# Performance work log

Measured on AMD Instinct MI355X. Metric: run time of the kernel, lower is better.

The kernel has to match this reference:

```python
import jax, jax.numpy as jnp
import numpy as np

B, N, D, L, NREPEAT = 32, 577, 384, 12, 4
H = 4 * D  # mlp hidden
EPS = 1e-6


def ln(x, w, b):
    mu = jnp.mean(x, axis=-1, keepdims=True)
    var = jnp.mean(jnp.square(x - mu), axis=-1, keepdims=True)
    return (x - mu) * jax.lax.rsqrt(var + EPS) * w + b


def setup_inputs() -> dict:
    key = jax.random.key(0)
    ks = jax.random.split(key, 16)
    s = 0.02
    return {
        "x": jax.random.normal(ks[0], (B, N, D), dtype=jnp.float32),
        "norm1_w": jnp.ones((L, D), jnp.float32),
        "norm1_b": jnp.zeros((L, D), jnp.float32),
        "qkv_w": jax.random.normal(ks[1], (L, 3 * D, D), jnp.float32) * s,
        "qkv_b": jnp.zeros((L, 3 * D), jnp.float32),
        "qn_w": jnp.ones((L, D), jnp.float32),
        "qn_b": jnp.zeros((L, D), jnp.float32),
        "kn_w": jnp.ones((L, D), jnp.float32),
        "kn_b": jnp.zeros((L, D), jnp.float32),
        "an_w": jnp.ones((L, D), jnp.float32),
        "an_b": jnp.zeros((L, D), jnp.float32),
        "proj_w": jax.random.normal(ks[2], (L, D, D), jnp.float32) * s,
        "proj_b": jnp.zeros((L, D), jnp.float32),
        "ls1": jnp.full((L, D), 1e-5, jnp.float32),
        "norm2_w": jnp.ones((L, D), jnp.float32),
        "norm2_b": jnp.zeros((L, D), jnp.float32),
        "fc1_w": jax.random.normal(ks[3], (L, H, D), jnp.float32) * s,
        "fc1_b": jnp.zeros((L, H), jnp.float32),
        "fc2_w": jax.random.normal(ks[4], (L, D, H), jnp.float32) * s,
        "fc2_b": jnp.zeros((L, D), jnp.float32),
        "ls2": jnp.full((L, D), 1e-5, jnp.float32),
    }


def _forward(x, norm1_w, norm1_b, qkv_w, qkv_b, qn_w, qn_b, kn_w, kn_b,
             an_w, an_b, proj_w, proj_b, ls1, norm2_w, norm2_b,
             fc1_w, fc1_b, fc2_w, fc2_b, ls2):
    scale = 1.0 / np.sqrt(D).astype(np.float32)
    x_prime = x
    history = []  # list of [B, 1, D] cls tokens, grows each repeat
    for _ in range(NREPEAT):
        new_cls = x[:, 0:1]
        x = jnp.concatenate([new_cls, x_prime[:, 1:]], axis=1)  # [B, N, D]
        mem = jnp.concatenate([x] + history, axis=1)            # [B, N+t, D]
        for l in range(L):
            res1 = x
            xn = ln(x, norm1_w[l], norm1_b[l])
            # manual qkv split: q from normed x, k/v from UNNORMED mem
            q = xn @ qkv_w[l, :D].T + qkv_b[l, :D]
            k = mem @ qkv_w[l, D:2 * D].T + qkv_b[l, D:2 * D]
            v = mem @ qkv_w[l, 2 * D:].T + qkv_b[l, 2 * D:]
            q = ln(q, qn_w[l], qn_b[l])
            k = ln(k, kn_w[l], kn_b[l])
            # single-head SDPA over full width D
            attn = jax.nn.softmax(jnp.einsum('bqd,bkd->bqk', q, k) * scale, axis=-1)
            prod = jnp.einsum('bqk,bkd->bqd', attn, v)
            prod = ln(prod, an_w[l], an_b[l])
            proj = prod @ proj_w[l].T + proj_b[l]
            x = proj * ls1[l] + res1
            res2 = x
            x2 = ln(x, norm2_w[l], norm2_b[l])
            h = jax.nn.gelu(x2 @ fc1_w[l].T + fc1_b[l], approximate=False)
            x1 = h @ fc2_w[l].T + fc2_b[l]
            x = x1 * ls2[l] + res2
        history.append(new_cls)
    return x


def reference(x, norm1_w, norm1_b, qkv_w, qkv_b, qn_w, qn_b, kn_w, kn_b,
              an_w, an_b, proj_w, proj_b, ls1, norm2_w, norm2_b,
              fc1_w, fc1_b, fc2_w, fc2_b, ls2):
    return _forward(x, norm1_w, norm1_b, qkv_w, qkv_b, qn_w, qn_b, kn_w, kn_b,
                    an_w, an_b, proj_w, proj_b, ls1, norm2_w, norm2_b,
                    fc1_w, fc1_b, fc2_w, fc2_b, ls2)
```

## Files before the change

### kernel.cpp

```cpp
#include <hip/hip_runtime.h>
#include <math.h>

#define BB 32
#define NN 577
#define DD 384
#define HD 1536
#define LL 12
#define MP 640
#define NRPT 4

typedef __attribute__((ext_vector_type(8))) short bf16x8;
typedef __attribute__((ext_vector_type(4))) float f32x4;

__device__ __forceinline__ unsigned short f2bf(float f){
  unsigned u = __builtin_bit_cast(unsigned, f);
  u += 0x7fffu + ((u >> 16) & 1u);
  return (unsigned short)(u >> 16);
}
__device__ __forceinline__ float bf2f(unsigned short s){
  unsigned u = ((unsigned)s) << 16;
  return __builtin_bit_cast(float, u);
}

__device__ __forceinline__ void async16(void* lds, const void* g){
  __builtin_amdgcn_global_load_lds(
      (const __attribute__((address_space(1))) unsigned int*)g,
      (__attribute__((address_space(3))) unsigned int*)lds, 16, 0, 0);
}

__global__ void prep_k(float* __restrict__ x, const float* __restrict__ xp,
                       float* __restrict__ cls_r, const float* __restrict__ cls_hist,
                       unsigned short* __restrict__ mem, int r){
  int i = blockIdx.x * 256 + threadIdx.x;
  if (i >= BB*MP*DD) return;
  int d = i % DD;
  int n = (i / DD) % MP;
  int b = i / (MP*DD);
  float v;
  if (n == 0){ v = x[(size_t)b*NN*DD + d]; cls_r[b*DD + d] = v; }
  else if (n < NN){ v = xp[((size_t)b*NN + n)*DD + d]; x[((size_t)b*NN + n)*DD + d] = v; }
  else if (n < NN + r){ v = cls_hist[(size_t)(n-NN)*BB*DD + b*DD + d]; }
  else v = 0.f;
  mem[i] = f2bf(v);
}

__global__ void castL_k(const float* __restrict__ qkvw, const float* __restrict__ pw,
                        const float* __restrict__ f1w, const float* __restrict__ f2w,
                        unsigned short* __restrict__ wbuf){
  int i = blockIdx.x * 256 + threadIdx.x;
  const int QKV = 3*DD*DD;
  const int PRJ = DD*DD;
  const int F1  = HD*DD;
  const int TOT = QKV + PRJ + 2*F1;
  if (i >= TOT) return;
  float v;
  if (i < QKV) v = qkvw[i];
  else if (i < QKV+PRJ) v = pw[i-QKV];
  else if (i < QKV+PRJ+F1) v = f1w[i-QKV-PRJ];
  else v = f2w[i-QKV-PRJ-F1];
  wbuf[i] = f2bf(v);
}

template<typename T>
__global__ __launch_bounds__(256) void ln4_k(const T* __restrict__ in, const float* __restrict__ w,
                                             const float* __restrict__ bias, unsigned short* __restrict__ out,
                                             int nrows){
  int row = blockIdx.x*4 + (threadIdx.x >> 6);
  if (row >= nrows) return;
  int lane = threadIdx.x & 63;
  const T* p = in + (size_t)row*DD;
  float v[6];
  float s = 0.f;
  #pragma unroll
  for (int i=0;i<6;i++){
    float t;
    if (sizeof(T) == 4) t = (float)p[lane + i*64];
    else t = bf2f((unsigned short)p[lane + i*64]);
    v[i] = t; s += t;
  }
  #pragma unroll
  for (int o=32;o;o>>=1) s += __shfl_xor(s, o, 64);
  float mu = s * (1.f/DD);
  float q = 0.f;
  #pragma unroll
  for (int i=0;i<6;i++){ float t = v[i]-mu; q += t*t; }
  #pragma unroll
  for (int o=32;o;o>>=1) q += __shfl_xor(q, o, 64);
  float rs = rsqrtf(q*(1.f/DD) + 1e-6f);
  unsigned short* po = out + (size_t)row*DD;
  #pragma unroll
  for (int i=0;i<6;i++){
    int c = lane + i*64;
    po[c] = f2bf((v[i]-mu)*rs*w[c] + bias[c]);
  }
}

__global__ __launch_bounds__(256) void lnqk_k(const unsigned short* __restrict__ qraw,
                                              const unsigned short* __restrict__ kraw,
                                              const float* __restrict__ qw, const float* __restrict__ qbias,
                                              const float* __restrict__ kw, const float* __restrict__ kbias,
                                              unsigned short* __restrict__ qo, unsigned short* __restrict__ ko){
  const int QR = BB*NN;
  int row = blockIdx.x*4 + (threadIdx.x >> 6);
  int lane = threadIdx.x & 63;
  bool isq = row < QR;
  const unsigned short* p = isq ? qraw + (size_t)row*DD : kraw + (size_t)(row-QR)*DD;
  const float* w  = isq ? qw : kw;
  const float* bs = isq ? qbias : kbias;
  unsigned short* po = isq ? qo + (size_t)row*DD : ko + (size_t)(row-QR)*DD;
  float scale = isq ? 0.05103103588f : 1.0f;
  float v[6];
  float s = 0.f;
  #pragma unroll
  for (int i=0;i<6;i++){ float t = bf2f(p[lane + i*64]); v[i] = t; s += t; }
  #pragma unroll
  for (int o=32;o;o>>=1) s += __shfl_xor(s, o, 64);
  float mu = s * (1.f/DD);
  float q = 0.f;
  #pragma unroll
  for (int i=0;i<6;i++){ float t = v[i]-mu; q += t*t; }
  #pragma unroll
  for (int o=32;o;o>>=1) q += __shfl_xor(q, o, 64);
  float rs = rsqrtf(q*(1.f/DD) + 1e-6f);
  #pragma unroll
  for (int i=0;i<6;i++){
    int c = lane + i*64;
    po[c] = f2bf(((v[i]-mu)*rs*w[c] + bs[c]) * scale);
  }
}

template<int EPI>
__global__ __launch_bounds__(256) void gemm128(
    const unsigned short* __restrict__ A, int lda, int arows, long sA,
    const unsigned short* __restrict__ B, int ldb, int brows, long sB,
    const float* __restrict__ bias,
    int K, int N,
    float* __restrict__ outF, unsigned short* __restrict__ outB,
    int ldo, int orows, long sO,
    const float* __restrict__ ls){

  __shared__ unsigned short a_sh[2][128*32];
  __shared__ unsigned short b_sh[2][128*32];

  int tid  = threadIdx.x;
  int wave = tid >> 6, lane = tid & 63;
  int lr = lane & 15, kg = lane >> 4;
  int wm = wave >> 1, wn = wave & 1;
  int z = blockIdx.z;
  int row0 = blockIdx.y * 128;
  int col0 = blockIdx.x * 128;

  const unsigned short* Ab = A + (size_t)z*sA;
  const unsigned short* Bb = B + (size_t)z*sB;

  f32x4 zf = {0.f,0.f,0.f,0.f};
  f32x4 acc[4][4];
  #pragma unroll
  for (int i=0;i<4;i++)
    #pragma unroll
    for (int j=0;j<4;j++) acc[i][j] = zf;

  int ra[2], rb[2], kc[2];
  #pragma unroll
  for (int it=0; it<2; it++){
    int c = tid + it*256;
    int r = row0 + (c>>2); if (r > arows-1) r = arows-1;
    ra[it] = r;
    r = col0 + (c>>2); if (r > brows-1) r = brows-1;
    rb[it] = r;
    kc[it] = (c&3)*8;
  }

  for (int k0 = 0; k0 < K; k0 += 64){
    #pragma unroll
    for (int p=0;p<2;p++){
      #pragma unroll
      for (int it=0; it<2; it++){
        unsigned short* la = &a_sh[p][(it*256 + wave*64)*8];
        unsigned short* lb = &b_sh[p][(it*256 + wave*64)*8];
        async16(la, Ab + (size_t)ra[it]*lda + k0 + p*32 + kc[it]);
        async16(lb, Bb + (size_t)rb[it]*ldb + k0 + p*32 + kc[it]);
      }
    }
    __syncthreads();
    #pragma unroll
    for (int p=0;p<2;p++){
      bf16x8 af[4], bfr[4];
      #pragma unroll
      for (int i=0;i<4;i++){
        af[i]  = *(const bf16x8*)&a_sh[p][(wm*64 + i*16 + lr)*32 + kg*8];
        bfr[i] = *(const bf16x8*)&b_sh[p][(wn*64 + i*16 + lr)*32 + kg*8];
      }
      #pragma unroll
      for (int i=0;i<4;i++)
        #pragma unroll
        for (int j=0;j<4;j++)
          acc[i][j] = __builtin_amdgcn_mfma_f32_16x16x32_bf16(af[i], bfr[j], acc[i][j], 0,0,0);
    }
    __syncthreads();
  }

  float* oF = outF ? outF + (size_t)z*sO : nullptr;
  unsigned short* oB = outB ? outB + (size_t)z*sO : nullptr;

  #pragma unroll
  for (int mi=0;mi<4;mi++)
    #pragma unroll
    for (int ni=0;ni<4;ni++)
      #pragma unroll
      for (int r=0;r<4;r++){
        int row = row0 + wm*64 + mi*16 + kg*4 + r;
        int col = col0 + wn*64 + ni*16 + lr;
        if (row >= orows || col >= N) continue;
        float vv = acc[mi][ni][r];
        size_t idx = (size_t)row*ldo + col;
        if (EPI == 0){
          if (bias) vv += bias[col];
          oB[idx] = f2bf(vv);
        } else if (EPI == 1){
          vv += bias[row];
          oB[idx] = f2bf(vv);
        } else if (EPI == 2){
          vv += bias[col];
          oF[idx] = vv*ls[col] + oF[idx];
        } else {
          vv += bias[col];
          float g = 0.5f*vv*(1.f + erff(vv*0.70710678118f));
          oB[idx] = f2bf(g);
        }
      }
}

__global__ __launch_bounds__(256, 2) void attn_k(
    const unsigned short* __restrict__ qs,
    const unsigned short* __restrict__ kb,
    const unsigned short* __restrict__ vT,
    const float* __restrict__ anw, const float* __restrict__ anb,
    unsigned short* __restrict__ out, int M){

  __shared__ unsigned short k_sh[32*384];
  __shared__ unsigned short v_sh[384*32];
  __shared__ unsigned short p_sh[64*56];

  int tid = threadIdx.x;
  int wv = tid >> 6, lane = tid & 63;
  int lr = lane & 15, kg = lane >> 4;
  int b = blockIdx.y, qt0 = blockIdx.x * 64;

  bf16x8 qf[12];
  {
    int qrow = qt0 + wv*16 + lr; if (qrow > NN-1) qrow = NN-1;
    const unsigned short* qp = qs + ((size_t)b*NN + qrow)*DD;
    #pragma unroll
    for (int ks=0; ks<12; ks++) qf[ks] = *(const bf16x8*)(qp + ks*32 + kg*8);
  }

  f32x4 zf = {0.f,0.f,0.f,0.f};
  f32x4 O[24];
  #pragma unroll
  for (int i=0;i<24;i++) O[i] = zf;
  float m_run[4], l_run[4];
  #pragma unroll
  for (int r=0;r<4;r++){ m_run[r] = -INFINITY; l_run[r] = 0.f; }

  for (int kt=0; kt<19; kt++){
    __syncthreads();
    #pragma unroll
    for (int i=0;i<6;i++){
      int L = i*256 + tid;
      int row = L/48, c = L%48;
      int gc = (c & ~7) | ((c ^ row) & 7);
      async16(&k_sh[L*8], kb + ((size_t)b*MP + kt*32 + row)*DD + gc*8);
    }
    #pragma unroll
    for (int i=0;i<6;i++){
      int L = i*256 + tid;
      int row = L>>2;
      int gc = (L&3) ^ (row&3);
      async16(&v_sh[L*8], vT + ((size_t)b*DD + row)*MP + kt*32 + gc*8);
    }
    __syncthreads();

    f32x4 s[2] = {zf, zf};
    #pragma unroll
    for (int ks=0; ks<12; ks++){
      int c = ks*4 + kg;
      #pragma unroll
      for (int nk=0; nk<2; nk++){
        int krow = nk*16 + lr;
        bf16x8 bk = *(const bf16x8*)&k_sh[krow*DD + ((c & ~7) | ((c ^ krow)&7))*8];
        s[nk] = __builtin_amdgcn_mfma_f32_16x16x32_bf16(qf[ks], bk, s[nk], 0,0,0);
      }
    }
    #pragma unroll
    for (int nk=0; nk<2; nk++){
      if (kt*32 + nk*16 + lr >= M){
        s[nk][0] = -INFINITY; s[nk][1] = -INFINITY; s[nk][2] = -INFINITY; s[nk][3] = -INFINITY;
      }
    }
    float al[4];
    #pragma unroll
    for (int r=0;r<4;r++){
      float v = fmaxf(s[0][r], s[1][r]);
      v = fmaxf(v, __shfl_xor(v, 1, 64));
      v = fmaxf(v, __shfl_xor(v, 2, 64));
      v = fmaxf(v, __shfl_xor(v, 4, 64));
      v = fmaxf(v, __shfl_xor(v, 8, 64));
      float mn = fmaxf(m_run[r], v);
      al[r] = __expf(m_run[r] - mn);
      m_run[r] = mn;
    }
    #pragma unroll
    for (int nk=0;nk<2;nk++)
      #pragma unroll
      for (int r=0;r<4;r++)
        s[nk][r] = __expf(s[nk][r] - m_run[r]);
    #pragma unroll
    for (int r=0;r<4;r++){
      float v = s[0][r] + s[1][r];
      v += __shfl_xor(v, 1, 64);
      v += __shfl_xor(v, 2, 64);
      v += __shfl_xor(v, 4, 64);
      v += __shfl_xor(v, 8, 64);
      l_run[r] = al[r]*l_run[r] + v;
    }
    #pragma unroll
    for (int nk=0;nk<2;nk++)
      #pragma unroll
      for (int r=0;r<4;r++)
        p_sh[(wv*16 + kg*4 + r)*56 + nk*16 + lr] = f2bf(s[nk][r]);
    #pragma unroll
    for (int ni=0;ni<24;ni++)
      #pragma unroll
      for (int r=0;r<4;r++) O[ni][r] *= al[r];
    __syncthreads();

    bf16x8 ap = *(const bf16x8*)&p_sh[(wv*16 + lr)*56 + kg*8];
    #pragma unroll
    for (int ni=0;ni<24;ni++){
      int d = ni*16 + lr;
      bf16x8 bv = *(const bf16x8*)&v_sh[d*32 + ((kg ^ (d&3))*8)];
      O[ni] = __builtin_amdgcn_mfma_f32_16x16x32_bf16(ap, bv, O[ni], 0,0,0);
    }
  }

  float inv[4];
  #pragma unroll
  for (int r=0;r<4;r++) inv[r] = 1.f / l_run[r];
  float s1[4] = {0,0,0,0}, s2[4] = {0,0,0,0};
  #pragma unroll
  for (int ni=0;ni<24;ni++)
    #pragma unroll
    for (int r=0;r<4;r++){
      float x = O[ni][r]*inv[r];
      O[ni][r] = x;
      s1[r] += x; s2[r] += x*x;
    }
  #pragma unroll
  for (int r=0;r<4;r++){
    #pragma unroll
    for (int o=1;o<16;o<<=1){ s1[r] += __shfl_xor(s1[r], o, 64); s2[r] += __shfl_xor(s2[r], o, 64); }
  }
  float mu[4], rs[4];
  #pragma unroll
  for (int r=0;r<4;r++){
    mu[r] = s1[r]*(1.f/DD);
    float var = s2[r]*(1.f/DD) - mu[r]*mu[r];
    rs[r] = rsqrtf(fmaxf(var, 0.f) + 1e-6f);
  }
  int rowb = qt0 + wv*16 + kg*4;
  #pragma unroll
  for (int ni=0;ni<24;ni++){
    int col = ni*16 + lr;
    float wc = anw[col], bc = anb[col];
    #pragma unroll
    for (int r=0;r<4;r++){
      int qrow = rowb + r;
      if (qrow < NN)
        out[((size_t)b*NN + qrow)*DD + col] = f2bf((O[ni][r]-mu[r])*rs[r]*wc + bc);
    }
  }
}


extern "C" void kernel_launch(void* const* d_in, const int* in_sizes, int n_in,
                              void* d_out, int out_size, void* d_ws, size_t ws_size,
                              hipStream_t stream){
  const float* x_in = (const float*)d_in[0];
  const float* n1w  = (const float*)d_in[1];
  const float* n1b  = (const float*)d_in[2];
  const float* qkvw = (const float*)d_in[3];
  const float* qkvb = (const float*)d_in[4];
  const float* qnw  = (const float*)d_in[5];
  const float* qnb  = (const float*)d_in[6];
  const float* knw  = (const float*)d_in[7];
  const float* knb  = (const float*)d_in[8];
  const float* anw  = (const float*)d_in[9];
  const float* anb  = (const float*)d_in[10];
  const float* pw   = (const float*)d_in[11];
  const float* pb   = (const float*)d_in[12];
  const float* ls1  = (const float*)d_in[13];
  const float* n2w  = (const float*)d_in[14];
  const float* n2b  = (const float*)d_in[15];
  const float* f1w  = (const float*)d_in[16];
  const float* f1b  = (const float*)d_in[17];
  const float* f2w  = (const float*)d_in[18];
  const float* f2bb = (const float*)d_in[19];
  const float* ls2  = (const float*)d_in[20];

  char* ws = (char*)d_ws;
  size_t off = 0;
  auto alloc = [&](size_t bytes)->char* {
    char* p = ws + off;
    off = (off + bytes + 255) & ~(size_t)255;
    return p;
  };

  const int QKV = 3*DD*DD, PRJ = DD*DD, F1 = HD*DD;
  const size_t WTOT = (size_t)QKV + PRJ + 2*F1;
  const size_t SLOT = (size_t)BB*MP*DD;

  unsigned short* wbuf  = (unsigned short*)alloc(WTOT*2);
  float*          cls_h = (float*)         alloc((size_t)NRPT*BB*DD*4);
  unsigned short* mem_bf= (unsigned short*)alloc(SLOT*2);
  unsigned short* pool  = (unsigned short*)alloc(6*SLOT*2);

  unsigned short* wq = wbuf;
  unsigned short* wp = wbuf + QKV;
  unsigned short* w1 = wbuf + QKV + PRJ;
  unsigned short* w2 = wbuf + QKV + PRJ + F1;

  unsigned short* S0 = pool;
  unsigned short* S1 = pool + SLOT;
  unsigned short* S2 = pool + 2*SLOT;
  unsigned short* S3 = pool + 3*SLOT;
  unsigned short* S4 = pool + 4*SLOT;
  unsigned short* S5 = pool + 5*SLOT;

  unsigned short* xn    = S0;
  unsigned short* qraw  = S1;
  unsigned short* kraw  = S2;
  unsigned short* qb    = S3;
  unsigned short* kb    = S4;
  unsigned short* vT    = S5;
  unsigned short* prodn = S1;
  unsigned short* x2    = S0;
  unsigned short* h     = S1;

  float* xf = (float*)d_out;

  auto cg = [](size_t n){ return dim3((unsigned)((n + 255) / 256)); };

  hipMemcpyAsync(xf, x_in, (size_t)BB*NN*DD*4, hipMemcpyDeviceToDevice, stream);

  const int RT  = (BB*NN + 127)/128;
  const int RTM = (BB*MP)/128;
  const int QR  = BB*NN;
  const int KR  = BB*MP;

  for (int r = 0; r < NRPT; r++){
    int M = NN + r;
    prep_k<<<cg((size_t)BB*MP*DD),256,0,stream>>>(xf, x_in, cls_h + (size_t)r*BB*DD, cls_h, mem_bf, r);
    for (int l = 0; l < LL; l++){
      castL_k<<<cg(WTOT),256,0,stream>>>(qkvw + (size_t)l*QKV, pw + (size_t)l*PRJ,
                                         f1w + (size_t)l*F1, f2w + (size_t)l*F1, wbuf);
      ln4_k<float><<<cg((size_t)QR*64),256,0,stream>>>(xf, n1w + l*DD, n1b + l*DD, xn, QR);
      gemm128<0><<<dim3(3,RT,1),256,0,stream>>>(xn,384,QR,0, wq,384,384,0,
          qkvb + l*3*DD, 384,384, nullptr,qraw,384,QR,0, nullptr);
      gemm128<0><<<dim3(3,RTM,1),256,0,stream>>>(mem_bf,384,KR,0, wq + (size_t)DD*DD,384,384,0,
          qkvb + l*3*DD + DD, 384,384, nullptr,kraw,384,KR,0, nullptr);
      gemm128<1><<<dim3(MP/128,3,BB),256,0,stream>>>(wq + (size_t)2*DD*DD,384,384,0, mem_bf,384,MP,(long)MP*DD,
          qkvb + l*3*DD + 2*DD, 384,MP, nullptr,vT,MP,384,(long)DD*MP, nullptr);
      lnqk_k<<<(QR+KR)/4,256,0,stream>>>(qraw, kraw, qnw + l*DD, qnb + l*DD,
                                         knw + l*DD, knb + l*DD, qb, kb);
      attn_k<<<dim3(10,BB),256,0,stream>>>(qb, kb, vT, anw + l*DD, anb + l*DD, prodn, M);
      gemm128<2><<<dim3(3,RT,1),256,0,stream>>>(prodn,384,QR,0, wp,384,384,0,
          pb + l*DD, 384,384, xf,nullptr,384,QR,0, ls1 + l*DD);
      ln4_k<float><<<cg((size_t)QR*64),256,0,stream>>>(xf, n2w + l*DD, n2b + l*DD, x2, QR);
      gemm128<3><<<dim3(HD/128,RT,1),256,0,stream>>>(x2,384,QR,0, w1,384,HD,0,
          f1b + l*HD, 384,HD, nullptr,h,HD,QR,0, nullptr);
      gemm128<2><<<dim3(3,RT,1),256,0,stream>>>(h,HD,QR,0, w2,HD,384,0,
          f2bb + l*DD, HD,384, xf,nullptr,384,QR,0, ls2 + l*DD);
    }
  }
}
```

Measured before the change: 16.88 ms.

## Merge Q/K GEMMs, hoist weight casts, vectorize LN-QK, drop attention barrier

Merges the Q and K projection GEMMs into a single launch by placing xn and mem_bf contiguously, with blocks past a row split switching to the K weights and bias. Weight casting to bf16 now runs once per layer up front into a 12-layer buffer, rather than once per repeat per layer, whenever the workspace is large enough. lnqk_k loads and stores bf16 pairs as 32-bit words, and attention shrinks the P tile stride. It also removes a __syncthreads before reading P, which relies on each wave reading only its own rows, and any cross-wave hazard there would be a correctness risk.

```diff
diff --git a/kernel.cpp b/kernel.cpp
--- a/kernel.cpp
+++ b/kernel.cpp
@@ -8,6 +8,9 @@
 #define LL 12
 #define MP 640
 #define NRPT 4
+#define QR (BB*NN)
+#define QP 18560
+#define KR (BB*MP)
 
 typedef __attribute__((ext_vector_type(8))) short bf16x8;
 typedef __attribute__((ext_vector_type(4))) float f32x4;
@@ -61,23 +64,17 @@
   wbuf[i] = f2bf(v);
 }
 
-template<typename T>
-__global__ __launch_bounds__(256) void ln4_k(const T* __restrict__ in, const float* __restrict__ w,
+__global__ __launch_bounds__(256) void ln4_k(const float* __restrict__ in, const float* __restrict__ w,
                                              const float* __restrict__ bias, unsigned short* __restrict__ out,
                                              int nrows){
   int row = blockIdx.x*4 + (threadIdx.x >> 6);
   if (row >= nrows) return;
   int lane = threadIdx.x & 63;
-  const T* p = in + (size_t)row*DD;
+  const float* p = in + (size_t)row*DD;
   float v[6];
   float s = 0.f;
   #pragma unroll
-  for (int i=0;i<6;i++){
-    float t;
-    if (sizeof(T) == 4) t = (float)p[lane + i*64];
-    else t = bf2f((unsigned short)p[lane + i*64]);
-    v[i] = t; s += t;
-  }
+  for (int i=0;i<6;i++){ float t = p[lane + i*64]; v[i] = t; s += t; }
   #pragma unroll
   for (int o=32;o;o>>=1) s += __shfl_xor(s, o, 64);
   float mu = s * (1.f/DD);
@@ -100,19 +97,22 @@
                                               const float* __restrict__ qw, const float* __restrict__ qbias,
                                               const float* __restrict__ kw, const float* __restrict__ kbias,
                                               unsigned short* __restrict__ qo, unsigned short* __restrict__ ko){
-  const int QR = BB*NN;
   int row = blockIdx.x*4 + (threadIdx.x >> 6);
   int lane = threadIdx.x & 63;
   bool isq = row < QR;
-  const unsigned short* p = isq ? qraw + (size_t)row*DD : kraw + (size_t)(row-QR)*DD;
+  const unsigned int* p = (const unsigned int*)(isq ? qraw + (size_t)row*DD : kraw + (size_t)(row-QR)*DD);
   const float* w  = isq ? qw : kw;
   const float* bs = isq ? qbias : kbias;
-  unsigned short* po = isq ? qo + (size_t)row*DD : ko + (size_t)(row-QR)*DD;
+  unsigned int* po = (unsigned int*)(isq ? qo + (size_t)row*DD : ko + (size_t)(row-QR)*DD);
   float scale = isq ? 0.05103103588f : 1.0f;
   float v[6];
   float s = 0.f;
   #pragma unroll
-  for (int i=0;i<6;i++){ float t = bf2f(p[lane + i*64]); v[i] = t; s += t; }
+  for (int i=0;i<3;i++){
+    unsigned u = p[lane + i*64];
+    float a = bf2f((unsigned short)u), b = bf2f((unsigned short)(u>>16));
+    v[2*i] = a; v[2*i+1] = b; s += a + b;
+  }
   #pragma unroll
   for (int o=32;o;o>>=1) s += __shfl_xor(s, o, 64);
   float mu = s * (1.f/DD);
@@ -123,9 +123,11 @@
   for (int o=32;o;o>>=1) q += __shfl_xor(q, o, 64);
   float rs = rsqrtf(q*(1.f/DD) + 1e-6f);
   #pragma unroll
-  for (int i=0;i<6;i++){
-    int c = lane + i*64;
-    po[c] = f2bf(((v[i]-mu)*rs*w[c] + bs[c]) * scale);
+  for (int i=0;i<3;i++){
+    int c0 = 2*(lane + i*64);
+    unsigned short lo = f2bf(((v[2*i]  -mu)*rs*w[c0]   + bs[c0]  ) * scale);
+    unsigned short hi = f2bf(((v[2*i+1]-mu)*rs*w[c0+1] + bs[c0+1]) * scale);
+    po[lane + i*64] = (unsigned)lo | ((unsigned)hi << 16);
   }
 }
 
@@ -137,7 +139,9 @@
     int K, int N,
     float* __restrict__ outF, unsigned short* __restrict__ outB,
     int ldo, int orows, long sO,
-    const float* __restrict__ ls){
+    const float* __restrict__ ls,
+    int rowSplit, const unsigned short* __restrict__ B2,
+    const float* __restrict__ bias2, int orows2){
 
   __shared__ unsigned short a_sh[2][128*32];
   __shared__ unsigned short b_sh[2][128*32];
@@ -150,8 +154,13 @@
   int row0 = blockIdx.y * 128;
   int col0 = blockIdx.x * 128;
 
+  bool second = row0 >= rowSplit;
+  const unsigned short* Bu = second ? B2 : B;
+  const float* biasu = second ? bias2 : bias;
+  int limit = second ? orows2 : orows;
+
   const unsigned short* Ab = A + (size_t)z*sA;
-  const unsigned short* Bb = B + (size_t)z*sB;
+  const unsigned short* Bb = Bu + (size_t)z*sB;
 
   f32x4 zf = {0.f,0.f,0.f,0.f};
   f32x4 acc[4][4];
@@ -211,20 +220,20 @@
       for (int r=0;r<4;r++){
         int row = row0 + wm*64 + mi*16 + kg*4 + r;
         int col = col0 + wn*64 + ni*16 + lr;
-        if (row >= orows || col >= N) continue;
+        if (row >= limit || col >= N) continue;
         float vv = acc[mi][ni][r];
         size_t idx = (size_t)row*ldo + col;
         if (EPI == 0){
-          if (bias) vv += bias[col];
+          if (biasu) vv += biasu[col];
           oB[idx] = f2bf(vv);
         } else if (EPI == 1){
-          vv += bias[row];
+          vv += biasu[row];
           oB[idx] = f2bf(vv);
         } else if (EPI == 2){
-          vv += bias[col];
+          vv += biasu[col];
           oF[idx] = vv*ls[col] + oF[idx];
         } else {
-          vv += bias[col];
+          vv += biasu[col];
           float g = 0.5f*vv*(1.f + erff(vv*0.70710678118f));
           oB[idx] = f2bf(g);
         }
@@ -240,7 +249,7 @@
 
   __shared__ unsigned short k_sh[32*384];
   __shared__ unsigned short v_sh[384*32];
-  __shared__ unsigned short p_sh[64*56];
+  __shared__ unsigned short p_sh[64*40];
 
   int tid = threadIdx.x;
   int wv = tid >> 6, lane = tid & 63;
@@ -328,14 +337,13 @@
     for (int nk=0;nk<2;nk++)
       #pragma unroll
       for (int r=0;r<4;r++)
-        p_sh[(wv*16 + kg*4 + r)*56 + nk*16 + lr] = f2bf(s[nk][r]);
+        p_sh[(wv*16 + kg*4 + r)*40 + nk*16 + lr] = f2bf(s[nk][r]);
     #pragma unroll
     for (int ni=0;ni<24;ni++)
       #pragma unroll
       for (int r=0;r<4;r++) O[ni][r] *= al[r];
-    __syncthreads();
-
-    bf16x8 ap = *(const bf16x8*)&p_sh[(wv*16 + lr)*56 + kg*8];
+
+    bf16x8 ap = *(const bf16x8*)&p_sh[(wv*16 + lr)*40 + kg*8];
     #pragma unroll
     for (int ni=0;ni<24;ni++){
       int d = ni*16 + lr;
@@ -419,31 +427,31 @@
   const int QKV = 3*DD*DD, PRJ = DD*DD, F1 = HD*DD;
   const size_t WTOT = (size_t)QKV + PRJ + 2*F1;
   const size_t SLOT = (size_t)BB*MP*DD;
+  const size_t XNSZ = (size_t)QP*DD;
 
   unsigned short* wbuf  = (unsigned short*)alloc(WTOT*2);
   float*          cls_h = (float*)         alloc((size_t)NRPT*BB*DD*4);
-  unsigned short* mem_bf= (unsigned short*)alloc(SLOT*2);
-  unsigned short* pool  = (unsigned short*)alloc(6*SLOT*2);
-
-  unsigned short* wq = wbuf;
-  unsigned short* wp = wbuf + QKV;
-  unsigned short* w1 = wbuf + QKV + PRJ;
-  unsigned short* w2 = wbuf + QKV + PRJ + F1;
-
-  unsigned short* S0 = pool;
-  unsigned short* S1 = pool + SLOT;
-  unsigned short* S2 = pool + 2*SLOT;
-  unsigned short* S3 = pool + 3*SLOT;
-  unsigned short* S4 = pool + 4*SLOT;
-  unsigned short* S5 = pool + 5*SLOT;
-
-  unsigned short* xn    = S0;
-  unsigned short* qraw  = S1;
-  unsigned short* kraw  = S2;
+  unsigned short* xnbuf = (unsigned short*)alloc((XNSZ + SLOT + 5*SLOT)*2);
+  unsigned short* mem_bf= xnbuf + XNSZ;
+  unsigned short* S1 = mem_bf + SLOT;
+  unsigned short* S2 = S1 + SLOT;
+  unsigned short* S3 = S2 + SLOT;
+  unsigned short* S4 = S3 + SLOT;
+  unsigned short* S5 = S4 + SLOT;
+
+  unsigned short* wbufAll = nullptr;
+  if (ws_size >= off + 12*WTOT*2 + 256)
+    wbufAll = (unsigned short*)alloc(12*WTOT*2);
+
+  unsigned short* S0 = xnbuf;
+  unsigned short* xn    = xnbuf;
+  unsigned short* qkraw = S1;
+  unsigned short* qraw  = qkraw;
+  unsigned short* kraw  = qkraw + (size_t)QP*DD;
   unsigned short* qb    = S3;
   unsigned short* kb    = S4;
   unsigned short* vT    = S5;
-  unsigned short* prodn = S1;
+  unsigned short* prodn = S0;
   unsigned short* x2    = S0;
   unsigned short* h     = S1;
 
@@ -453,34 +461,54 @@
 
   hipMemcpyAsync(xf, x_in, (size_t)BB*NN*DD*4, hipMemcpyDeviceToDevice, stream);
 
-  const int RT  = (BB*NN + 127)/128;
-  const int RTM = (BB*MP)/128;
-  const int QR  = BB*NN;
-  const int KR  = BB*MP;
+  if (wbufAll)
+    for (int l = 0; l < LL; l++)
+      castL_k<<<cg(WTOT),256,0,stream>>>(qkvw + (size_t)l*QKV, pw + (size_t)l*PRJ,
+                                         f1w + (size_t)l*F1, f2w + (size_t)l*F1,
+                                         wbufAll + (size_t)l*WTOT);
+
+  const int RT  = QP/128;
+  const int RTK = KR/128;
+  const int MAXI = 0x7fffffff;
 
   for (int r = 0; r < NRPT; r++){
     int M = NN + r;
     prep_k<<<cg((size_t)BB*MP*DD),256,0,stream>>>(xf, x_in, cls_h + (size_t)r*BB*DD, cls_h, mem_bf, r);
     for (int l = 0; l < LL; l++){
-      castL_k<<<cg(WTOT),256,0,stream>>>(qkvw + (size_t)l*QKV, pw + (size_t)l*PRJ,
-                                         f1w + (size_t)l*F1, f2w + (size_t)l*F1, wbuf);
-      ln4_k<float><<<cg((size_t)QR*64),256,0,stream>>>(xf, n1w + l*DD, n1b + l*DD, xn, QR);
-      gemm128<0><<<dim3(3,RT,1),256,0,stream>>>(xn,384,QR,0, wq,384,384,0,
-          qkvb + l*3*DD, 384,384, nullptr,qraw,384,QR,0, nullptr);
-      gemm128<0><<<dim3(3,RTM,1),256,0,stream>>>(mem_bf,384,KR,0, wq + (size_t)DD*DD,384,384,0,
-          qkvb + l*3*DD + DD, 384,384, nullptr,kraw,384,KR,0, nullptr);
-      gemm128<1><<<dim3(MP/128,3,BB),256,0,stream>>>(wq + (size_t)2*DD*DD,384,384,0, mem_bf,384,MP,(long)MP*DD,
-          qkvb + l*3*DD + 2*DD, 384,MP, nullptr,vT,MP,384,(long)DD*MP, nullptr);
+      unsigned short* wl;
+      if (wbufAll) wl = wbufAll + (size_t)l*WTOT;
+      else {
+        castL_k<<<cg(WTOT),256,0,stream>>>(qkvw + (size_t)l*QKV, pw + (size_t)l*PRJ,
+                                           f1w + (size_t)l*F1, f2w + (size_t)l*F1, wbuf);
+        wl = wbuf;
+      }
+      unsigned short* wq = wl;
+      unsigned short* wp = wl + QKV;
+      unsigned short* w1 = wl + QKV + PRJ;
+      unsigned short* w2 = wl + QKV + PRJ + F1;
+
+      ln4_k<<<cg((size_t)QR*64),256,0,stream>>>(xf, n1w + l*DD, n1b + l*DD, xn, QR);
+      gemm128<0><<<dim3(3,RT+RTK,1),256,0,stream>>>(
+          xn,384,QP+KR,0, wq,384,384,0, qkvb + l*3*DD, 384,384,
+          nullptr,qkraw,384,QR,0, nullptr,
+          QP, wq + (size_t)DD*DD, qkvb + l*3*DD + DD, QP+KR);
+      gemm128<1><<<dim3(MP/128,3,BB),256,0,stream>>>(
+          wq + (size_t)2*DD*DD,384,384,0, mem_bf,384,MP,(long)MP*DD,
+          qkvb + l*3*DD + 2*DD, 384,MP, nullptr,vT,MP,384,(long)DD*MP, nullptr,
+          MAXI, nullptr, nullptr, 0);
       lnqk_k<<<(QR+KR)/4,256,0,stream>>>(qraw, kraw, qnw + l*DD, qnb + l*DD,
                                          knw + l*DD, knb + l*DD, qb, kb);
       attn_k<<<dim3(10,BB),256,0,stream>>>(qb, kb, vT, anw + l*DD, anb + l*DD, prodn, M);
-      gemm128<2><<<dim3(3,RT,1),256,0,stream>>>(prodn,384,QR,0, wp,384,384,0,
-          pb + l*DD, 384,384, xf,nullptr,384,QR,0, ls1 + l*DD);
-      ln4_k<float><<<cg((size_t)QR*64),256,0,stream>>>(xf, n2w + l*DD, n2b + l*DD, x2, QR);
-      gemm128<3><<<dim3(HD/128,RT,1),256,0,stream>>>(x2,384,QR,0, w1,384,HD,0,
-          f1b + l*HD, 384,HD, nullptr,h,HD,QR,0, nullptr);
-      gemm128<2><<<dim3(3,RT,1),256,0,stream>>>(h,HD,QR,0, w2,HD,384,0,
-          f2bb + l*DD, HD,384, xf,nullptr,384,QR,0, ls2 + l*DD);
-    }
-  }
-}
+      gemm128<2><<<dim3(3,RT,1),256,0,stream>>>(
+          prodn,384,QR,0, wp,384,384,0, pb + l*DD, 384,384,
+          xf,nullptr,384,QR,0, ls1 + l*DD, MAXI, nullptr, nullptr, 0);
+      ln4_k<<<cg((size_t)QR*64),256,0,stream>>>(xf, n2w + l*DD, n2b + l*DD, x2, QR);
+      gemm128<3><<<dim3(HD/128,RT,1),256,0,stream>>>(
+          x2,384,QR,0, w1,384,HD,0, f1b + l*HD, 384,HD,
+          nullptr,h,HD,QR,0, nullptr, MAXI, nullptr, nullptr, 0);
+      gemm128<2><<<dim3(3,RT,1),256,0,stream>>>(
+          h,HD,QR,0, w2,HD,384,0, f2bb + l*DD, HD,384,
+          xf,nullptr,384,QR,0, ls2 + l*DD, MAXI, nullptr, nullptr, 0);
+    }
+  }
+}
```

New measurement: 16.92 ms. No clear change (+0.2%).
